# Optimization experiments

Measured on AMD Instinct MI355X. Metric: run time of the kernel, lower is better.

Reference implementation:

```python
import jax, jax.numpy as jnp
import numpy as np

EPS_BN = 1e-5
DIVERSITY_TEMP = 100.0  # lucidrains codebook_diversity_temperature default
COMMIT_W = 1.0
DIVERSITY_W = 1.0
ORTHO_W = 1.0


def conv1d(x, w, b=None, stride=1, pad=0):
    # x: [B,C,T], w: [O,I,K] (torch layout)
    y = jax.lax.conv_general_dilated(x, w, (stride,), [(pad, pad)],
                                     dimension_numbers=('NCH', 'OIH', 'NCH'))
    if b is not None:
        y = y + b[None, :, None]
    return y


def conv1d_transpose(x, w_torch, stride, pad):
    # torch ConvTranspose1d weight: (in, out, k). Equivalent input-dilated conv
    # with flipped kernel and padding k-1-pad.
    w = jnp.flip(jnp.transpose(w_torch, (1, 0, 2)), axis=2)  # -> (out,in,k)
    k = w.shape[2]
    p = k - 1 - pad
    return jax.lax.conv_general_dilated(x, w, (1,), [(p, p)],
                                        lhs_dilation=(stride,),
                                        dimension_numbers=('NCH', 'OIH', 'NCH'))


def batchnorm(x, g, b):
    # training-mode BatchNorm1d: stats over (batch, time) per channel
    m = x.mean(axis=(0, 2), keepdims=True)
    v = x.var(axis=(0, 2), keepdims=True)
    return (x - m) * jax.lax.rsqrt(v + EPS_BN) * g[None, :, None] + b[None, :, None]


def setup_inputs():
    key = jax.random.key(0)
    ks = jax.random.split(key, 10)
    f32 = jnp.float32
    rn = lambda k, shape, s: jax.random.normal(k, shape, f32) * s
    return {
        'x': jax.random.normal(ks[0], (8, 1, 24000), f32),
        # encoder: 1->16->32->64
        'w1': rn(ks[1], (16, 1, 5), 0.3), 'b1': jnp.zeros(16, f32),
        'g1': jnp.ones(16, f32), 'be1': jnp.zeros(16, f32),
        'w2': rn(ks[2], (32, 16, 5), 0.1), 'b2': jnp.zeros(32, f32),
        'g2': jnp.ones(32, f32), 'be2': jnp.zeros(32, f32),
        'w3': rn(ks[3], (64, 32, 25), 0.05), 'b3': jnp.zeros(64, f32),
        'g3': jnp.ones(64, f32), 'be3': jnp.zeros(64, f32),
        # VQ codebook [codebook_size=8192, dim=64]
        'embed': jax.random.normal(ks[4], (8192, 64), f32),
        # decoder
        'dw1': rn(ks[5], (64, 64, 25), 0.05),  # ConvTranspose1d weight (in,out,k)
        'dg1': jnp.ones(64, f32), 'dbe1': jnp.zeros(64, f32),
        'dw2': rn(ks[6], (64, 64, 5), 0.1), 'db2': jnp.zeros(64, f32),
        'dg2': jnp.ones(64, f32), 'dbe2': jnp.zeros(64, f32),
        'dw3': rn(ks[7], (1, 64, 1), 0.2), 'db3': jnp.zeros(1, f32),
        # fixed random subset for orthogonal reg (orthogonal_reg_max_codes=256)
        'ortho_idx': jax.random.randint(ks[8], (256,), 0, 8192),
    }


def reference(x, w1, b1, g1, be1, w2, b2, g2, be2, w3, b3, g3, be3,
              embed, dw1, dg1, dbe1, dw2, db2, dg2, dbe2, dw3, db3, ortho_idx):
    # ---- encoder ----
    h = batchnorm(jax.nn.silu(conv1d(x, w1, b1, 1, 2)), g1, be1)
    h = batchnorm(jax.nn.silu(conv1d(h, w2, b2, 1, 2)), g2, be2)
    z = batchnorm(jnp.tanh(conv1d(h, w3, b3, 12, 12)), g3, be3)  # [B,64,N]
    B, C, N = z.shape
    zf = jnp.transpose(z, (0, 2, 1)).reshape(B * N, C)  # [B*N, 64]

    # ---- VQ: nearest neighbor over codebook ----
    d2 = (jnp.sum(zf * zf, -1, keepdims=True) - 2.0 * (zf @ embed.T)
          + jnp.sum(embed * embed, -1)[None, :])          # [B*N, K]
    dist = jnp.sqrt(jnp.clip(d2, 1e-12))                  # euclidean (cdist p=2)
    idx = jnp.argmin(d2, axis=-1)                         # [B*N]
    q = embed[idx]                                        # codebook gather

    commit = jnp.mean((jax.lax.stop_gradient(q) - zf) ** 2)

    prob = jax.nn.softmax(-dist * DIVERSITY_TEMP, axis=-1)
    avg_prob = prob.mean(axis=0)                          # [K]
    diversity = jnp.sum(avg_prob * jnp.log(jnp.clip(avg_prob, 1e-30)))

    codes = embed[ortho_idx]                              # [256, 64]
    normed = codes * jax.lax.rsqrt(jnp.sum(codes * codes, -1, keepdims=True) + 1e-12)
    cos = normed @ normed.T
    n = codes.shape[0]
    ortho = jnp.sum(cos * cos) / (n * n) - 1.0 / n

    loss = COMMIT_W * commit + DIVERSITY_W * diversity + ORTHO_W * ortho

    # straight-through estimator
    q_st = zf + jax.lax.stop_gradient(q - zf)
    zq = jnp.transpose(q_st.reshape(B, N, C), (0, 2, 1))  # [B,64,N]

    # ---- decoder ----
    d = batchnorm(jax.nn.silu(conv1d_transpose(zq, dw1, 12, 12)), dg1, dbe1)
    d = batchnorm(jax.nn.silu(conv1d(d, dw2, db2, 1, 2)), dg2, dbe2)
    recon = conv1d(d, dw3, db3, 1, 0)

    T = x.shape[2]
    cur = recon.shape[2]
    if cur > T:
        recon = recon[:, :, :T]
    elif cur < T:
        recon = jnp.pad(recon, ((0, 0), (0, 0), (0, T - cur)))
    return recon, idx.reshape(B, N), loss, (commit, diversity, ortho)
```

## Files before the change

### kernel.cpp

```cpp
#include <hip/hip_runtime.h>
#include <math.h>
#include <float.h>

#define DEV __device__ __forceinline__

#define BB 8
#define TT 24000
#define TD 23989
#define NZ 2000
#define ROWS 16000
#define NE 8192
#define NCG 8

typedef __attribute__((ext_vector_type(8))) short bf16x8;
typedef __attribute__((ext_vector_type(4))) float f32x4;

__device__ double g_st[640];
__device__ double g_misc[2];
__device__ float  g_e2[NE];
__device__ float  g_avg[NE];
__device__ float  g_z2[ROWS];
__device__ float  g_rdm[ROWS];
__device__ int    g_rix[ROWS];
__device__ float  g_ob[256 * 64];
__device__ float  g_pmd[ROWS * NCG];
__device__ int    g_pmi[ROWS * NCG];
__device__ int    g_pcc[ROWS * NCG];
__device__ float2 g_cand[ROWS * 256];
__device__ unsigned short g_zbh[ROWS * 64], g_zbl[ROWS * 64];
__device__ unsigned short g_ebh[NE * 64],  g_ebl[NE * 64];
__device__ float  g_s1[16], g_sh1[16];
__device__ float  g_s2[32], g_sh2[32];
__device__ float  g_sd1[64], g_shd1[64];
__device__ float  g_w2f[2560];
__device__ float  g_b2f[32];
__device__ float  g_w3f[64 * 32 * 25];
__device__ float  g_b3f[64];
__device__ float  g_dw2f[64 * 5 * 64];
__device__ float  g_db2f[64];
__device__ float  g_dw1t[64 * 64 * 25];
__device__ float  g_zbn[ROWS * 64];
__device__ double g_zbnd[ROWS * 64];
__device__ float  g_zq[BB * 64 * NZ];
__device__ float  g_y1[BB * 16 * TT];
__device__ float  g_zpre[BB * 64 * NZ];
__device__ float  g_yd1[BB * 64 * TD];
__device__ float  g_y2[BB * 32 * TT];
__device__ float  g_yd2[BB * 64 * TD];

DEV float wsum(float v){
  #pragma unroll
  for (int o = 32; o; o >>= 1) v += __shfl_xor(v, o, 64);
  return v;
}
DEV int clampc(int c){ return c < 0 ? 0 : (c > NE - 1 ? NE - 1 : c); }
DEV float bss(unsigned short s){ union { unsigned u; float f; } v; v.u = ((unsigned)s) << 16; return v.f; }
DEV unsigned short f2bs(float f){
  union { float f; unsigned u; } v; v.f = f;
  unsigned r = (v.u + 0x7FFF + ((v.u >> 16) & 1)) >> 16;
  return (unsigned short)r;
}

__global__ void k_zero(){
  int i = blockIdx.x * 256 + threadIdx.x;
  if (i < 640) g_st[i] = 0.0;
  if (i < 2) g_misc[i] = 0.0;
  if (i < NE) g_avg[i] = 0.f;
}

__global__ void k_embprep(const float* __restrict__ embed){
  int gt = blockIdx.x * 256 + threadIdx.x;
  int gs = gridDim.x * 256;
  for (int i = gt; i < NE * 64; i += gs){
    float v = embed[i];
    unsigned short h = f2bs(v);
    g_ebh[i] = h;
    g_ebl[i] = f2bs(v - bss(h));
  }
  for (int c = gt; c < NE; c += gs){
    float s = 0.f;
    for (int j = 0; j < 64; j++){ float v = embed[c * 64 + j]; s += v * v; }
    g_e2[c] = s;
  }
}

__global__ void k_zsplit(){
  int i = blockIdx.x * 256 + threadIdx.x;
  if (i < ROWS * 64){
    float v = g_zbn[i];
    unsigned short h = f2bs(v);
    g_zbh[i] = h;
    g_zbl[i] = f2bs(v - bss(h));
  }
}

__global__ void k_conv1(const float* __restrict__ x, const float* __restrict__ w1,
                        const float* __restrict__ b1){
  int b = blockIdx.y, t0 = blockIdx.x * 256, tid = threadIdx.x;
  __shared__ float xs[260], wl[80], bl[16], sacc[16], qacc[16];
  if (tid < 80) wl[tid] = w1[tid];
  if (tid < 16){ bl[tid] = b1[tid]; sacc[tid] = 0.f; qacc[tid] = 0.f; }
  for (int i = tid; i < 260; i += 256){ int g = t0 - 2 + i; xs[i] = ((unsigned)g < TT) ? x[b * TT + g] : 0.f; }
  __syncthreads();
  int t = t0 + tid;
  bool ok = t < TT;
  float xv[5];
  #pragma unroll
  for (int k = 0; k < 5; k++) xv[k] = xs[tid + k];
  float out[16];
  #pragma unroll
  for (int c = 0; c < 16; c++){
    float a = bl[c];
    #pragma unroll
    for (int k = 0; k < 5; k++) a += wl[c * 5 + k] * xv[k];
    float o = ok ? a / (1.f + expf(-a)) : 0.f;
    out[c] = o;
    if (ok) g_y1[(b * 16 + c) * TT + t] = o;
  }
  int lane = tid & 63;
  #pragma unroll
  for (int c = 0; c < 16; c++){
    float s = wsum(out[c]);
    float q = wsum(out[c] * out[c]);
    if (lane == 0){ atomicAdd(&sacc[c], s); atomicAdd(&qacc[c], q); }
  }
  __syncthreads();
  if (tid < 16){ atomicAdd(&g_st[tid * 2], (double)sacc[tid]); atomicAdd(&g_st[tid * 2 + 1], (double)qacc[tid]); }
}

__global__ void k_fold2(const float* __restrict__ g1, const float* __restrict__ be1,
                        const float* __restrict__ w2, const float* __restrict__ b2){
  int tid = threadIdx.x;
  if (blockIdx.x == 0 && tid < 16){
    double m = g_st[tid * 2] / 192000.0, v = g_st[tid * 2 + 1] / 192000.0 - m * m;
    float s = g1[tid] / sqrtf((float)v + 1e-5f);
    g_s1[tid] = s; g_sh1[tid] = be1[tid] - (float)m * s;
  }
  if (blockIdx.x == 0 && tid < 32) g_b2f[tid] = b2[tid];
  int gt = blockIdx.x * 256 + tid;
  for (int i = gt; i < 2560; i += 8 * 256){
    int co = i & 31, r = i >> 5, k = r % 5, ci = r / 5;
    g_w2f[i] = w2[(co * 16 + ci) * 5 + k];
  }
}

__global__ void __launch_bounds__(256) k_conv2(){
  int b = blockIdx.y, t0 = blockIdx.x * 256, tid = threadIdx.x;
  __shared__ float xs[16][260];
  __shared__ float sacc[32], qacc[32];
  __shared__ float s1l[16], sh1l[16];
  int lane = tid & 63, wv = tid >> 6;
  int cb = wv * 8;
  if (tid < 32){ sacc[tid] = 0.f; qacc[tid] = 0.f; }
  if (tid < 16){ s1l[tid] = g_s1[tid]; sh1l[tid] = g_sh1[tid]; }
  __syncthreads();
  for (int i = tid; i < 16 * 260; i += 256){
    int ci = i / 260, tt = i - ci * 260, g = t0 - 2 + tt;
    xs[ci][tt] = ((unsigned)g < TT) ? (s1l[ci] * g_y1[(b * 16 + ci) * TT + g] + sh1l[ci]) : 0.f;
  }
  __syncthreads();
  float acc[4][8];
  #pragma unroll
  for (int j = 0; j < 4; j++)
    #pragma unroll
    for (int i = 0; i < 8; i++) acc[j][i] = g_b2f[cb + i];
  for (int ci = 0; ci < 16; ci++){
    #pragma unroll
    for (int k = 0; k < 5; k++){
      const float4* wp = (const float4*)(g_w2f + (ci * 5 + k) * 32 + cb);
      float4 w0 = wp[0], w1v = wp[1];
      float wr[8] = { w0.x, w0.y, w0.z, w0.w, w1v.x, w1v.y, w1v.z, w1v.w };
      #pragma unroll
      for (int j = 0; j < 4; j++){
        float xv = xs[ci][lane + 64 * j + k];
        #pragma unroll
        for (int i = 0; i < 8; i++) acc[j][i] += wr[i] * xv;
      }
    }
  }
  #pragma unroll
  for (int i = 0; i < 8; i++){
    int co = cb + i;
    float s = 0.f, q = 0.f;
    #pragma unroll
    for (int j = 0; j < 4; j++){
      int t = t0 + lane + 64 * j;
      bool ok = t < TT;
      float a = acc[j][i];
      float o = ok ? a / (1.f + expf(-a)) : 0.f;
      if (ok) g_y2[(b * 32 + co) * TT + t] = o;
      s += o; q += o * o;
    }
    s = wsum(s); q = wsum(q);
    if (lane == 0){ atomicAdd(&sacc[co], s); atomicAdd(&qacc[co], q); }
  }
  __syncthreads();
  if (tid < 32){ atomicAdd(&g_st[128 + tid * 2], (double)sacc[tid]); atomicAdd(&g_st[128 + tid * 2 + 1], (double)qacc[tid]); }
}

__global__ void k_fold3(const float* __restrict__ g2, const float* __restrict__ be2,
                        const float* __restrict__ w3, const float* __restrict__ b3){
  int tid = threadIdx.x;
  if (blockIdx.x == 0 && tid < 32){
    double m = g_st[128 + tid * 2] / 192000.0, v = g_st[128 + tid * 2 + 1] / 192000.0 - m * m;
    float s = g2[tid] / sqrtf((float)v + 1e-5f);
    g_s2[tid] = s; g_sh2[tid] = be2[tid] - (float)m * s;
  }
  if (blockIdx.x == 0 && tid >= 64 && tid < 128) g_b3f[tid - 64] = b3[tid - 64];
  int gt = blockIdx.x * 256 + tid;
  for (int i = gt; i < 64 * 32 * 25; i += 64 * 256){
    int co = i & 63, r = i >> 6, k = r % 25, ci = r / 25;
    g_w3f[i] = w3[(co * 32 + ci) * 25 + k];
  }
}

__global__ void __launch_bounds__(256) k_conv3(){
  __shared__ float xs[32][400];
  __shared__ float s2l[32], sh2l[32];
  int tid = threadIdx.x, b = blockIdx.y, t0 = blockIdx.x * 32;
  int lane = tid & 63, wv = tid >> 6;
  int cb = wv * 16;
  int tl = lane & 31, h = lane >> 5;
  if (tid < 32){ s2l[tid] = g_s2[tid]; sh2l[tid] = g_sh2[tid]; }
  __syncthreads();
  int p0 = t0 * 12 - 12;
  for (int i = tid; i < 32 * 397; i += 256){
    int ci = i / 397, pp = i - ci * 397, g = p0 + pp;
    xs[ci][pp] = ((unsigned)g < TT) ? (s2l[ci] * g_y2[(b * 32 + ci) * TT + g] + sh2l[ci]) : 0.f;
  }
  __syncthreads();
  float acc[16];
  #pragma unroll
  for (int i = 0; i < 16; i++) acc[i] = 0.f;
  for (int cii = 0; cii < 16; cii++){
    int ci = h * 16 + cii;
    #pragma unroll
    for (int k = 0; k < 25; k++){
      float xv = xs[ci][tl * 12 + k];
      const float4* wp = (const float4*)(g_w3f + (ci * 25 + k) * 64 + cb);
      float4 a0 = wp[0], a1 = wp[1], a2 = wp[2], a3 = wp[3];
      acc[0] += a0.x * xv; acc[1] += a0.y * xv; acc[2] += a0.z * xv; acc[3] += a0.w * xv;
      acc[4] += a1.x * xv; acc[5] += a1.y * xv; acc[6] += a1.z * xv; acc[7] += a1.w * xv;
      acc[8] += a2.x * xv; acc[9] += a2.y * xv; acc[10] += a2.z * xv; acc[11] += a2.w * xv;
      acc[12] += a3.x * xv; acc[13] += a3.y * xv; acc[14] += a3.z * xv; acc[15] += a3.w * xv;
    }
  }
  #pragma unroll
  for (int i = 0; i < 16; i++) acc[i] += __shfl_xor(acc[i], 32, 64);
  int t = t0 + tl;
  if (h == 0 && t < NZ){
    #pragma unroll
    for (int i = 0; i < 16; i++)
      g_zpre[(b * 64 + cb + i) * NZ + t] = tanhf(acc[i] + g_b3f[cb + i]);
  }
}

__global__ void k_stats(int which, int L, int stoff){
  const float* p = (which == 0) ? g_zpre : (which == 1) ? g_yd1 : g_yd2;
  int co = blockIdx.y, t0 = blockIdx.x * 256, tid = threadIdx.x;
  int t = t0 + tid;
  float s = 0.f, q = 0.f;
  if (t < L){
    for (int b = 0; b < BB; b++){ float v = p[(b * 64 + co) * L + t]; s += v; q += v * v; }
  }
  s = wsum(s); q = wsum(q);
  __shared__ float sa[4], qa[4];
  int w = tid >> 6, lane = tid & 63;
  if (lane == 0){ sa[w] = s; qa[w] = q; }
  __syncthreads();
  if (tid == 0){
    atomicAdd(&g_st[stoff + co * 2], (double)(sa[0] + sa[1] + sa[2] + sa[3]));
    atomicAdd(&g_st[stoff + co * 2 + 1], (double)(qa[0] + qa[1] + qa[2] + qa[3]));
  }
}

__global__ void k_zbn(const float* __restrict__ g3, const float* __restrict__ be3){
  __shared__ float tile[64][65];
  __shared__ float s3[64], sh3[64];
  __shared__ double s3d[64], sh3d[64];
  int tid = threadIdx.x, b = blockIdx.y, n0 = blockIdx.x * 64;
  if (tid < 64){
    double m = g_st[256 + tid * 2] / 16000.0, v = g_st[256 + tid * 2 + 1] / 16000.0 - m * m;
    double sd = (double)g3[tid] / sqrt(v + 1e-5);
    double shd = (double)be3[tid] - m * sd;
    s3d[tid] = sd; sh3d[tid] = shd;
    s3[tid] = (float)sd; sh3[tid] = (float)shd;
  }
  __syncthreads();
  for (int i = tid; i < 64 * 64; i += 256){
    int c = i >> 6, nn = i & 63, n = n0 + nn;
    tile[c][nn] = (n < NZ) ? (s3[c] * g_zpre[(b * 64 + c) * NZ + n] + sh3[c]) : 0.f;
  }
  __syncthreads();
  int lane = tid & 63;
  for (int it = 0; it < 16; ++it){
    int nn = (tid >> 6) + it * 4;
    int n = n0 + nn, c = lane;
    if (n < NZ){
      float v = tile[c][nn];
      int row = b * NZ + n;
      g_zbn[row * 64 + c] = v;
      g_zbnd[row * 64 + c] = s3d[c] * (double)g_zpre[(b * 64 + c) * NZ + n] + sh3d[c];
      float s = wsum(v * v);
      if (lane == 0) g_z2[row] = s;
    }
  }
}

__global__ void __launch_bounds__(256) k_vq1(){
  __shared__ unsigned short bsh[64 * 72];
  __shared__ unsigned short bsl[64 * 72];
  __shared__ float2 ring[64][16];
  __shared__ int cnt[64];
  int tid = threadIdx.x, lane = tid & 63, w = tid >> 6;
  int q = lane >> 4, col = lane & 15;
  int rowbase = blockIdx.x * 64 + w * 16;
  int cbase = blockIdx.y * 1024;
  int grp = blockIdx.y;
  if (tid < 64) cnt[tid] = 0;
  #pragma unroll
  for (int i = 0; i < 4; i++)
    ring[w * 16 + (lane & 15)][(lane >> 4) * 4 + i] = make_float2(FLT_MAX, __int_as_float(NE - 1));
  bf16x8 ah0, ah1, al0, al1;
  {
    const unsigned short* zh = g_zbh + (rowbase + col) * 64;
    const unsigned short* zl = g_zbl + (rowbase + col) * 64;
    ah0 = *(const bf16x8*)(zh + q * 8);
    ah1 = *(const bf16x8*)(zh + 32 + q * 8);
    al0 = *(const bf16x8*)(zl + q * 8);
    al1 = *(const bf16x8*)(zl + 32 + q * 8);
  }
  float z2r[4];
  #pragma unroll
  for (int r = 0; r < 4; r++) z2r[r] = g_z2[rowbase + q * 4 + r];
  float thr[4], lmin[4]; int lamc[4];
  #pragma unroll
  for (int r = 0; r < 4; r++){ thr[r] = FLT_MAX; lmin[r] = FLT_MAX; lamc[r] = NE - 1; }
  float runmin[4] = {FLT_MAX, FLT_MAX, FLT_MAX, FLT_MAX};
  for (int ch = 0; ch < 16; ++ch){
    __syncthreads();
    {
      int cl = tid >> 2, seg = tid & 3;
      int cglob = cbase + ch * 64 + cl;
      *(int4*)&bsh[cl * 72 + seg * 16]     = *(const int4*)(g_ebh + cglob * 64 + seg * 16);
      *(int4*)&bsh[cl * 72 + seg * 16 + 8] = *(const int4*)(g_ebh + cglob * 64 + seg * 16 + 8);
      *(int4*)&bsl[cl * 72 + seg * 16]     = *(const int4*)(g_ebl + cglob * 64 + seg * 16);
      *(int4*)&bsl[cl * 72 + seg * 16 + 8] = *(const int4*)(g_ebl + cglob * 64 + seg * 16 + 8);
    }
    __syncthreads();
    float d2s[4][4];
    float tmin[4] = {FLT_MAX, FLT_MAX, FLT_MAX, FLT_MAX};
    #pragma unroll
    for (int t = 0; t < 4; t++){
      int ct = cbase + ch * 64 + t * 16;
      const unsigned short* bhp = &bsh[(t * 16 + col) * 72];
      const unsigned short* blp = &bsl[(t * 16 + col) * 72];
      bf16x8 bh0 = *(const bf16x8*)(bhp + q * 8);
      bf16x8 bh1 = *(const bf16x8*)(bhp + 32 + q * 8);
      bf16x8 bl0 = *(const bf16x8*)(blp + q * 8);
      bf16x8 bl1 = *(const bf16x8*)(blp + 32 + q * 8);
      f32x4 acc = {0.f, 0.f, 0.f, 0.f};
      acc = __builtin_amdgcn_mfma_f32_16x16x32_bf16(al0, bh0, acc, 0, 0, 0);
      acc = __builtin_amdgcn_mfma_f32_16x16x32_bf16(al1, bh1, acc, 0, 0, 0);
      acc = __builtin_amdgcn_mfma_f32_16x16x32_bf16(ah0, bl0, acc, 0, 0, 0);
      acc = __builtin_amdgcn_mfma_f32_16x16x32_bf16(ah1, bl1, acc, 0, 0, 0);
      acc = __builtin_amdgcn_mfma_f32_16x16x32_bf16(ah0, bh0, acc, 0, 0, 0);
      acc = __builtin_amdgcn_mfma_f32_16x16x32_bf16(ah1, bh1, acc, 0, 0, 0);
      float e2c = g_e2[ct + col];
      #pragma unroll
      for (int r = 0; r < 4; r++){
        float d = z2r[r] + e2c - 2.f * acc[r];
        d2s[t][r] = d;
        if (d < lmin[r]){ lmin[r] = d; lamc[r] = ct + col; }
        tmin[r] = fminf(tmin[r], d);
      }
    }
    #pragma unroll
    for (int r = 0; r < 4; r++){
      float m = tmin[r];
      m = fminf(m, __shfl_xor(m, 1, 64));
      m = fminf(m, __shfl_xor(m, 2, 64));
      m = fminf(m, __shfl_xor(m, 4, 64));
      m = fminf(m, __shfl_xor(m, 8, 64));
      if (m < runmin[r]){
        runmin[r] = m;
        thr[r] = m + 0.71f * sqrtf(fmaxf(m, 0.f)) + 0.13f;
      }
    }
    #pragma unroll
    for (int t = 0; t < 4; t++){
      int ct = cbase + ch * 64 + t * 16;
      bool any = false;
      #pragma unroll
      for (int r = 0; r < 4; r++) if (d2s[t][r] < thr[r]) any = true;
      if (__ballot(any)){
        #pragma unroll
        for (int r = 0; r < 4; r++){
          if (d2s[t][r] < thr[r]){
            int lr = w * 16 + q * 4 + r;
            int s = atomicAdd(&cnt[lr], 1) & 15;
            ring[lr][s] = make_float2(sqrtf(fmaxf(d2s[t][r], 1e-12f)), __int_as_float(ct + col));
          }
        }
      }
    }
  }
  __syncthreads();
  #pragma unroll
  for (int r = 0; r < 4; r++){
    float m = lmin[r]; int c = lamc[r];
    #pragma unroll
    for (int o = 1; o <= 8; o <<= 1){
      float om = __shfl_xor(m, o, 64);
      int oc = __shfl_xor(c, o, 64);
      if (om < m || (om == m && oc < c)){ m = om; c = oc; }
    }
    if (col == 0){
      int gr = rowbase + q * 4 + r;
      g_pmd[gr * NCG + grp] = m;
      g_pmi[gr * NCG + grp] = c;
    }
  }
  if (lane < 16){
    int lr = w * 16 + lane;
    g_pcc[(rowbase + lane) * NCG + grp] = cnt[lr];
  }
  #pragma unroll
  for (int i = 0; i < 4; i++){
    int idx = lane * 4 + i;
    int lr = idx >> 4, s = idx & 15;
    g_cand[(rowbase + lr) * 256 + grp * 16 + s] = ring[w * 16 + lr][s];
  }
}

__global__ void k_vq1b(){
  int row = blockIdx.x * 256 + threadIdx.x;
  if (row >= ROWS) return;
  float best = FLT_MAX; int bi = NE - 1;
  for (int cg = 0; cg < NCG; ++cg){
    float d = g_pmd[row * NCG + cg]; int i = g_pmi[row * NCG + cg];
    if (d < best || (d == best && i < bi)){ best = d; bi = i; }
  }
  g_rdm[row] = sqrtf(fmaxf(best, 1e-12f));
  g_rix[row] = bi;
}

__global__ void __launch_bounds__(256) k_vq3(const float* __restrict__ embed,
                                             float* __restrict__ outIdx){
  __shared__ int   ccode[4][144];
  __shared__ float cdst[4][144];
  __shared__ int   cn[4];
  __shared__ double bsum[4];
  int w = threadIdx.x >> 6, lane = threadIdx.x & 63;
  int row = blockIdx.x * 4 + w;
  float dmin = g_rdm[row];
  int seedc = clampc(g_rix[row]);
  if (lane == 0){ cn[w] = 0; ccode[w][0] = seedc; }
  __syncthreads();
  if (lane == 0) cn[w] = 1;
  int grp = lane & 7;
  int sub = lane >> 3;
  int cnt = g_pcc[row * NCG + grp]; if (cnt > 16) cnt = 16;
  int s0 = sub * 2, s1 = s0 + 2; if (s1 > cnt) s1 = cnt;
  for (int s = s0; s < s1; ++s){
    float2 cd = g_cand[row * 256 + grp * 16 + s];
    float dist = cd.x; int c = clampc(__float_as_int(cd.y));
    if (dist <= dmin + 0.353f && c != seedc){
      int i = atomicAdd(&cn[w], 1);
      ccode[w][i] = c;
    }
  }
  __syncthreads();
  int n = cn[w];
  double zdl = g_zbnd[row * 64 + lane];
  double bd = DBL_MAX; int bc = NE - 1;
  for (int i = 0; i < n; i++){
    int c = ccode[w][i];
    double diff = zdl - (double)embed[c * 64 + lane];
    double d = diff * diff;
    #pragma unroll
    for (int o = 32; o; o >>= 1) d += __shfl_xor(d, o, 64);
    if (lane == 0) cdst[w][i] = (float)d;
    if (d < bd || (d == bd && c < bc)){ bd = d; bc = c; }
  }
  __syncthreads();
  float dminE = (float)sqrt(bd);
  float Zp = 0.f;
  for (int i = lane; i < n; i += 64)
    Zp += expf(-100.f * (sqrtf(cdst[w][i]) - dminE));
  float Z = fmaxf(wsum(Zp), 1e-30f);
  if (lane == 0){
    g_rix[row] = bc;
    outIdx[row] = (float)bc;
    bsum[w] = bd;
  }
  for (int i = lane; i < n; i += 64)
    atomicAdd(&g_avg[ccode[w][i]], expf(-100.f * (sqrtf(cdst[w][i]) - dminE)) / Z);
  __syncthreads();
  if (threadIdx.x == 0)
    atomicAdd(&g_misc[0], bsum[0] + bsum[1] + bsum[2] + bsum[3]);
}

__global__ void k_orthoprep(const float* __restrict__ embed, const int* __restrict__ oidx){
  int tid = threadIdx.x;
  int c = clampc(oidx[tid]);
  float s = 0.f;
  for (int j = 0; j < 64; j++){ float v = embed[c * 64 + j]; s += v * v; }
  float r = 1.f / sqrtf(s + 1e-12f);
  for (int j = 0; j < 64; j++) g_ob[tid * 64 + j] = embed[c * 64 + j] * r;
}

__global__ void k_ortho(){
  int w = threadIdx.x >> 6, lane = threadIdx.x & 63;
  int i = blockIdx.x * 4 + w;
  float acc = 0.f;
  for (int j = lane; j < 256; j += 64){
    float d = 0.f;
    for (int k = 0; k < 64; k++) d += g_ob[i * 64 + k] * g_ob[j * 64 + k];
    acc += d * d;
  }
  acc = wsum(acc);
  if (lane == 0) atomicAdd(&g_misc[1], (double)acc);
}

__global__ void k_div(float* __restrict__ outS){
  int tid = threadIdx.x;
  double part = 0.0;
  for (int c = tid; c < NE; c += 256){
    double p = (double)g_avg[c] / 16000.0;
    double pc = p < 1e-30 ? 1e-30 : p;
    part += p * log(pc);
  }
  __shared__ double red[256];
  red[tid] = part; __syncthreads();
  for (int o = 128; o; o >>= 1){ if (tid < o) red[tid] += red[tid + o]; __syncthreads(); }
  if (tid == 0){
    double diversity = red[0];
    double commit = g_misc[0] / (double)(ROWS * 64);
    double ortho = g_misc[1] / 65536.0 - 1.0 / 256.0;
    double loss = commit + diversity + ortho;
    outS[0] = (float)loss;
    outS[1] = (float)commit;
    outS[2] = (float)diversity;
    outS[3] = (float)ortho;
  }
}

__global__ void k_zq(const float* __restrict__ embed){
  __shared__ float tile[64][65];
  int tid = threadIdx.x, b = blockIdx.y, n0 = blockIdx.x * 64;
  for (int i = tid; i < 64 * 64; i += 256){
    int nn = i >> 6, c = i & 63;
    int n = n0 + nn;
    int code = (n < NZ) ? clampc(g_rix[b * NZ + n]) : 0;
    tile[c][nn] = embed[code * 64 + c];
  }
  __syncthreads();
  for (int i = tid; i < 64 * 64; i += 256){
    int c = i >> 6, nn = i & 63;
    int n = n0 + nn;
    if (n < NZ) g_zq[(b * 64 + c) * NZ + n] = tile[c][nn];
  }
}

__global__ void k_folddw1(const float* __restrict__ dw1){
  int gt = blockIdx.x * 256 + threadIdx.x;
  for (int i = gt; i < 64 * 64 * 25; i += 100 * 256){
    int co = i & 63, r = i >> 6, k = r % 25, ci = r / 25;
    g_dw1t[i] = dw1[(ci * 64 + co) * 25 + (24 - k)];
  }
}

__global__ void __launch_bounds__(256, 3) k_dconv1(){
  __shared__ float xsd[16][260];
  __shared__ float wsh[4][64][28];
  __shared__ float sacc[4], qacc[4];
  int tid = threadIdx.x, b = blockIdx.y;
  int cb = blockIdx.z * 4;
  int t0 = blockIdx.x * 3072;
  int nb = blockIdx.x * 256 - 1;
  int w = tid >> 6, lane = tid & 63;
  if (tid < 4){ sacc[tid] = 0.f; qacc[tid] = 0.f; }
  for (int i = tid; i < 6400; i += 256){
    int c = i & 3, r = i >> 2;
    int k = r % 25, ci = r / 25;
    wsh[c][ci][k] = g_dw1t[r * 64 + cb + c];
  }
  float acc[4][12];
  #pragma unroll
  for (int q = 0; q < 4; q++)
    #pragma unroll
    for (int p = 0; p < 12; p++) acc[q][p] = 0.f;
  for (int cc = 0; cc < 4; ++cc){
    __syncthreads();
    for (int i = tid; i < 16 * 259; i += 256){
      int ci = i / 259, nl = i - ci * 259;
      int n = nb + nl;
      xsd[ci][nl] = ((unsigned)n < NZ) ? g_zq[(b * 64 + cc * 16 + ci) * NZ + n] : 0.f;
    }
    __syncthreads();
    #pragma unroll 2
    for (int ci = 0; ci < 16; ++ci){
      int cia = cc * 16 + ci;
      const float4* xp = (const float4*)&xsd[ci][4 * lane];
      float4 xA = xp[0], xB = xp[1];
      float xv[6] = { xA.x, xA.y, xA.z, xA.w, xB.x, xB.y };
      const float4* wp = (const float4*)&wsh[w][cia][0];
      float4 w0 = wp[0], w1 = wp[1], w2 = wp[2], w3 = wp[3], w4 = wp[4], w5 = wp[5];
      float wv[25] = { w0.x, w0.y, w0.z, w0.w, w1.x, w1.y, w1.z, w1.w,
                       w2.x, w2.y, w2.z, w2.w, w3.x, w3.y, w3.z, w3.w,
                       w4.x, w4.y, w4.z, w4.w, w5.x, w5.y, w5.z, w5.w,
                       wsh[w][cia][24] };
      #pragma unroll
      for (int q = 0; q < 4; ++q){
        acc[q][0] += wv[0] * xv[q];
        acc[q][0] += wv[12] * xv[q + 1];
        acc[q][0] += wv[24] * xv[q + 2];
        #pragma unroll
        for (int p = 1; p < 12; ++p){
          acc[q][p] += wv[12 - p] * xv[q + 1];
          acc[q][p] += wv[24 - p] * xv[q + 2];
        }
      }
    }
  }
  bool full = (t0 + 3072 <= TD);
  float s = 0.f, qs = 0.f;
  float* dst = &g_yd1[(b * 64 + cb + w) * TD + t0 + lane * 48];
  #pragma unroll
  for (int q = 0; q < 4; ++q){
    float o[12];
    #pragma unroll
    for (int p = 0; p < 12; ++p){
      int t = t0 + lane * 48 + q * 12 + p;
      float a = acc[q][p];
      float v = (t < TD) ? a / (1.f + expf(-a)) : 0.f;
      o[p] = v; s += v; qs += v * v;
    }
    if (full){
      ((float4*)(dst + q * 12))[0] = make_float4(o[0], o[1], o[2], o[3]);
      ((float4*)(dst + q * 12))[1] = make_float4(o[4], o[5], o[6], o[7]);
      ((float4*)(dst + q * 12))[2] = make_float4(o[8], o[9], o[10], o[11]);
    } else {
      #pragma unroll
      for (int p = 0; p < 12; ++p){
        int t = t0 + lane * 48 + q * 12 + p;
        if (t < TD) dst[q * 12 + p] = o[p];
      }
    }
  }
  s = wsum(s); qs = wsum(qs);
  if (lane == 0){ atomicAdd(&sacc[w], s); atomicAdd(&qacc[w], qs); }
  __syncthreads();
  if (tid < 4){
    atomicAdd(&g_st[384 + (cb + tid) * 2], (double)sacc[tid]);
    atomicAdd(&g_st[384 + (cb + tid) * 2 + 1], (double)qacc[tid]);
  }
}

__global__ void k_foldd2(const float* __restrict__ dg1, const float* __restrict__ dbe1,
                         const float* __restrict__ dw2, const float* __restrict__ db2){
  int tid = threadIdx.x;
  if (blockIdx.x == 0 && tid < 64){
    double m = g_st[384 + tid * 2] / 191912.0, v = g_st[384 + tid * 2 + 1] / 191912.0 - m * m;
    float sc = dg1[tid] / sqrtf((float)v + 1e-5f);
    g_sd1[tid] = sc; g_shd1[tid] = dbe1[tid] - (float)m * sc;
    g_db2f[tid] = db2[tid];
  }
  int gt = blockIdx.x * 256 + tid;
  for (int i = gt; i < 64 * 5 * 64; i += 32 * 256){
    int co = i & 63, r = i >> 6, k = r % 5, ci = r / 5;
    g_dw2f[i] = dw2[(co * 64 + ci) * 5 + k];
  }
}

__global__ void __launch_bounds__(256, 2) k_dconv2(){
  __shared__ float xs[16][772];
  __shared__ float wch[16 * 5 * 32];
  __shared__ float sdl[64], shdl[64];
  __shared__ float sacc[32], qacc[32];
  int tid = threadIdx.x, b = blockIdx.y, bz = blockIdx.z;
  int t0 = blockIdx.x * 768;
  int lane = tid & 63, wv = tid >> 6;
  int cb = bz * 32 + wv * 8;
  if (tid < 64){ sdl[tid] = g_sd1[tid]; shdl[tid] = g_shd1[tid]; }
  if (tid < 32){ sacc[tid] = 0.f; qacc[tid] = 0.f; }
  float acc[12][8];
  #pragma unroll
  for (int j = 0; j < 12; j++)
    #pragma unroll
    for (int i = 0; i < 8; i++) acc[j][i] = g_db2f[cb + i];
  for (int ch = 0; ch < 4; ++ch){
    __syncthreads();
    for (int i = tid; i < 16 * 772; i += 256){
      int ci = i / 772, tt = i - ci * 772, g = t0 - 2 + tt;
      int cia = ch * 16 + ci;
      xs[ci][tt] = ((unsigned)g < TD) ? (sdl[cia] * g_yd1[(b * 64 + cia) * TD + g] + shdl[cia]) : 0.f;
    }
    for (int i = tid; i < 2560; i += 256){
      int r = i >> 5, c = i & 31;
      wch[i] = g_dw2f[(ch * 80 + r) * 64 + bz * 32 + c];
    }
    __syncthreads();
    for (int ci = 0; ci < 16; ++ci){
      float xv[3][8];
      #pragma unroll
      for (int j4 = 0; j4 < 3; ++j4){
        const float4* xp = (const float4*)&xs[ci][j4 * 256 + 4 * lane];
        float4 a = xp[0], bq = xp[1];
        xv[j4][0] = a.x;  xv[j4][1] = a.y;  xv[j4][2] = a.z;  xv[j4][3] = a.w;
        xv[j4][4] = bq.x; xv[j4][5] = bq.y; xv[j4][6] = bq.z; xv[j4][7] = bq.w;
      }
      #pragma unroll
      for (int k = 0; k < 5; ++k){
        const float4* wp = (const float4*)(wch + (ci * 5 + k) * 32 + wv * 8);
        float4 w0 = wp[0], w1 = wp[1];
        float wr[8] = { w0.x, w0.y, w0.z, w0.w, w1.x, w1.y, w1.z, w1.w };
        #pragma unroll
        for (int j4 = 0; j4 < 3; ++j4){
          #pragma unroll
          for (int jj = 0; jj < 4; ++jj){
            float xvv = xv[j4][jj + k];
            #pragma unroll
            for (int i = 0; i < 8; i++) acc[j4 * 4 + jj][i] += wr[i] * xvv;
          }
        }
      }
    }
  }
  bool full = (t0 + 768 <= TD);
  #pragma unroll
  for (int i = 0; i < 8; i++){
    int co = cb + i;
    float s = 0.f, q = 0.f;
    float* dst = &g_yd2[(b * 64 + co) * TD + t0 + lane * 4];
    #pragma unroll
    for (int j4 = 0; j4 < 3; ++j4){
      float o[4];
      #pragma unroll
      for (int jj = 0; jj < 4; ++jj){
        int t = t0 + j4 * 256 + lane * 4 + jj;
        float a = acc[j4 * 4 + jj][i];
        float v = (t < TD) ? a / (1.f + expf(-a)) : 0.f;
        o[jj] = v; s += v; q += v * v;
      }
      if (full){
        *(float4*)(dst + j4 * 256) = make_float4(o[0], o[1], o[2], o[3]);
      } else {
        #pragma unroll
        for (int jj = 0; jj < 4; ++jj){
          int t = t0 + j4 * 256 + lane * 4 + jj;
          if (t < TD) dst[j4 * 256 + jj] = o[jj];
        }
      }
    }
    s = wsum(s); q = wsum(q);
    if (lane == 0){ atomicAdd(&sacc[wv * 8 + i], s); atomicAdd(&qacc[wv * 8 + i], q); }
  }
  __syncthreads();
  if (tid < 32){
    int co = bz * 32 + tid;
    atomicAdd(&g_st[512 + co * 2], (double)sacc[tid]);
    atomicAdd(&g_st[512 + co * 2 + 1], (double)qacc[tid]);
  }
}

__global__ void k_recon(const float* __restrict__ dg2, const float* __restrict__ dbe2,
                        const float* __restrict__ dw3, const float* __restrict__ db3,
                        float* __restrict__ outR){
  __shared__ float wf[64];
  __shared__ float bsh2;
  int tid = threadIdx.x, b = blockIdx.y, t0 = blockIdx.x * 256;
  if (tid < 64){
    double m = g_st[512 + tid * 2] / 191912.0, v = g_st[512 + tid * 2 + 1] / 191912.0 - m * m;
    float sc = dg2[tid] / sqrtf((float)v + 1e-5f);
    float shv = dbe2[tid] - (float)m * sc;
    wf[tid] = dw3[tid] * sc;
    float contrib = wsum(dw3[tid] * shv);
    if (tid == 0) bsh2 = db3[0] + contrib;
  }
  __syncthreads();
  int t = t0 + tid;
  if (t < TT){
    if (t < TD){
      float a = bsh2;
      for (int ci = 0; ci < 64; ci++) a += wf[ci] * g_yd2[(b * 64 + ci) * TD + t];
      outR[b * TT + t] = a;
    } else {
      outR[b * TT + t] = 0.f;
    }
  }
}

extern "C" void kernel_launch(void* const* d_in, const int* in_sizes, int n_in,
                              void* d_out, int out_size, void* d_ws, size_t ws_size,
                              hipStream_t stream){
  (void)in_sizes; (void)n_in; (void)out_size; (void)d_ws; (void)ws_size;
  const float* x    = (const float*)d_in[0];
  const float* w1   = (const float*)d_in[1];
  const float* b1   = (const float*)d_in[2];
  const float* g1   = (const float*)d_in[3];
  const float* be1  = (const float*)d_in[4];
  const float* w2   = (const float*)d_in[5];
  const float* b2   = (const float*)d_in[6];
  const float* g2   = (const float*)d_in[7];
  const float* be2  = (const float*)d_in[8];
  const float* w3   = (const float*)d_in[9];
  const float* b3   = (const float*)d_in[10];
  const float* g3   = (const float*)d_in[11];
  const float* be3  = (const float*)d_in[12];
  const float* embed= (const float*)d_in[13];
  const float* dw1  = (const float*)d_in[14];
  const float* dg1  = (const float*)d_in[15];
  const float* dbe1 = (const float*)d_in[16];
  const float* dw2  = (const float*)d_in[17];
  const float* db2  = (const float*)d_in[18];
  const float* dg2  = (const float*)d_in[19];
  const float* dbe2 = (const float*)d_in[20];
  const float* dw3  = (const float*)d_in[21];
  const float* db3  = (const float*)d_in[22];
  const int* oidx   = (const int*)d_in[23];

  float* out    = (float*)d_out;
  float* outIdx = out + 192000;
  float* outS   = out + 208000;

  hipLaunchKernelGGL(k_zero, dim3(32), dim3(256), 0, stream);
  hipLaunchKernelGGL(k_embprep, dim3(64), dim3(256), 0, stream, embed);
  hipLaunchKernelGGL(k_conv1, dim3(94, 8), dim3(256), 0, stream, x, w1, b1);
  hipLaunchKernelGGL(k_fold2, dim3(8), dim3(256), 0, stream, g1, be1, w2, b2);
  hipLaunchKernelGGL(k_conv2, dim3(94, 8), dim3(256), 0, stream);
  hipLaunchKernelGGL(k_fold3, dim3(64), dim3(256), 0, stream, g2, be2, w3, b3);
  hipLaunchKernelGGL(k_conv3, dim3(63, 8), dim3(256), 0, stream);
  hipLaunchKernelGGL(k_stats, dim3(8, 64), dim3(256), 0, stream, 0, NZ, 256);
  hipLaunchKernelGGL(k_zbn, dim3(32, 8), dim3(256), 0, stream, g3, be3);
  hipLaunchKernelGGL(k_zsplit, dim3(4000), dim3(256), 0, stream);
  hipLaunchKernelGGL(k_vq1, dim3(250, 8), dim3(256), 0, stream);
  hipLaunchKernelGGL(k_vq1b, dim3(63), dim3(256), 0, stream);
  hipLaunchKernelGGL(k_vq3, dim3(4000), dim3(256), 0, stream, embed, outIdx);
  hipLaunchKernelGGL(k_orthoprep, dim3(1), dim3(256), 0, stream, embed, oidx);
  hipLaunchKernelGGL(k_ortho, dim3(64), dim3(256), 0, stream);
  hipLaunchKernelGGL(k_div, dim3(1), dim3(256), 0, stream, outS);
  hipLaunchKernelGGL(k_zq, dim3(32, 8), dim3(256), 0, stream, embed);
  hipLaunchKernelGGL(k_folddw1, dim3(100), dim3(256), 0, stream, dw1);
  hipLaunchKernelGGL(k_dconv1, dim3(8, 8, 16), dim3(256), 0, stream);
  hipLaunchKernelGGL(k_foldd2, dim3(32), dim3(256), 0, stream, dg1, dbe1, dw2, db2);
  hipLaunchKernelGGL(k_dconv2, dim3(32, 8, 2), dim3(256), 0, stream);
  hipLaunchKernelGGL(k_recon, dim3(94, 8), dim3(256), 0, stream, dg2, dbe2, dw3, db3, out);
}
```

Measured before the change: 862.2 us.

## Double-buffer k_dconv2 input and weight tiles with register prefetch

Restructures the decoder conv2 kernel so input channels are staged in chunks of 8 into two shared-memory buffers. The next chunk is loaded from global memory into registers while the current chunk is computed. This hides global load latency behind the FMA loop and drops one barrier per chunk. It adds 30 prefetch registers on top of a 96-float accumulator under launch_bounds(256,2), which risks spills or lower occupancy, and it doubles the number of chunk iterations.

```diff
diff --git a/kernel.cpp b/kernel.cpp
--- a/kernel.cpp
+++ b/kernel.cpp
@@ -675,8 +675,8 @@
 }
 
 __global__ void __launch_bounds__(256, 2) k_dconv2(){
-  __shared__ float xs[16][772];
-  __shared__ float wch[16 * 5 * 32];
+  __shared__ float xs[2][8][772];
+  __shared__ float wch[2][1280];
   __shared__ float sdl[64], shdl[64];
   __shared__ float sacc[32], qacc[32];
   int tid = threadIdx.x, b = blockIdx.y, bz = blockIdx.z;
@@ -685,35 +685,79 @@
   int cb = bz * 32 + wv * 8;
   if (tid < 64){ sdl[tid] = g_sd1[tid]; shdl[tid] = g_shd1[tid]; }
   if (tid < 32){ sacc[tid] = 0.f; qacc[tid] = 0.f; }
+  __syncthreads();
+
   float acc[12][8];
   #pragma unroll
   for (int j = 0; j < 12; j++)
     #pragma unroll
     for (int i = 0; i < 8; i++) acc[j][i] = g_db2f[cb + i];
-  for (int ch = 0; ch < 4; ++ch){
-    __syncthreads();
-    for (int i = tid; i < 16 * 772; i += 256){
-      int ci = i / 772, tt = i - ci * 772, g = t0 - 2 + tt;
-      int cia = ch * 16 + ci;
-      xs[ci][tt] = ((unsigned)g < TD) ? (sdl[cia] * g_yd1[(b * 64 + cia) * TD + g] + shdl[cia]) : 0.f;
-    }
-    for (int i = tid; i < 2560; i += 256){
+
+  bool okj[3];
+  #pragma unroll
+  for (int j = 0; j < 3; j++) okj[j] = (unsigned)(t0 - 2 + tid + 256 * j) < TD;
+  int ecia_l = tid >> 2;
+  int eg = t0 - 2 + 768 + (tid & 3);
+  bool oke = (unsigned)eg < TD;
+
+  float pfx[25];
+  float pfw[5];
+
+  auto PREF = [&](int hc){
+    #pragma unroll
+    for (int ci = 0; ci < 8; ++ci){
+      const float* rowp = g_yd1 + (size_t)(b * 64 + hc * 8 + ci) * TD;
+      #pragma unroll
+      for (int j = 0; j < 3; ++j){
+        int g = t0 - 2 + tid + 256 * j;
+        pfx[ci * 3 + j] = rowp[okj[j] ? g : 0];
+      }
+    }
+    if (tid < 32)
+      pfx[24] = g_yd1[(size_t)(b * 64 + hc * 8 + ecia_l) * TD + (oke ? eg : 0)];
+    #pragma unroll
+    for (int j = 0; j < 5; ++j){
+      int i = tid + 256 * j;
       int r = i >> 5, c = i & 31;
-      wch[i] = g_dw2f[(ch * 80 + r) * 64 + bz * 32 + c];
-    }
-    __syncthreads();
-    for (int ci = 0; ci < 16; ++ci){
+      pfw[j] = g_dw2f[(hc * 40 + r) * 64 + bz * 32 + c];
+    }
+  };
+  auto WRITE = [&](int buf, int hc){
+    #pragma unroll
+    for (int ci = 0; ci < 8; ++ci){
+      int cia = hc * 8 + ci;
+      float s = sdl[cia], sh = shdl[cia];
+      #pragma unroll
+      for (int j = 0; j < 3; ++j)
+        xs[buf][ci][tid + 256 * j] = okj[j] ? (s * pfx[ci * 3 + j] + sh) : 0.f;
+    }
+    if (tid < 32){
+      int cia = hc * 8 + ecia_l;
+      xs[buf][ecia_l][768 + (tid & 3)] = oke ? (sdl[cia] * pfx[24] + shdl[cia]) : 0.f;
+    }
+    #pragma unroll
+    for (int j = 0; j < 5; ++j)
+      wch[buf][tid + 256 * j] = pfw[j];
+  };
+
+  PREF(0);
+  WRITE(0, 0);
+  __syncthreads();
+  for (int hc = 0; hc < 8; ++hc){
+    int cur = hc & 1;
+    if (hc < 7) PREF(hc + 1);
+    for (int ci = 0; ci < 8; ++ci){
       float xv[3][8];
       #pragma unroll
       for (int j4 = 0; j4 < 3; ++j4){
-        const float4* xp = (const float4*)&xs[ci][j4 * 256 + 4 * lane];
+        const float4* xp = (const float4*)&xs[cur][ci][j4 * 256 + 4 * lane];
         float4 a = xp[0], bq = xp[1];
         xv[j4][0] = a.x;  xv[j4][1] = a.y;  xv[j4][2] = a.z;  xv[j4][3] = a.w;
         xv[j4][4] = bq.x; xv[j4][5] = bq.y; xv[j4][6] = bq.z; xv[j4][7] = bq.w;
       }
       #pragma unroll
       for (int k = 0; k < 5; ++k){
-        const float4* wp = (const float4*)(wch + (ci * 5 + k) * 32 + wv * 8);
+        const float4* wp = (const float4*)(&wch[cur][(ci * 5 + k) * 32 + wv * 8]);
         float4 w0 = wp[0], w1 = wp[1];
         float wr[8] = { w0.x, w0.y, w0.z, w0.w, w1.x, w1.y, w1.z, w1.w };
         #pragma unroll
@@ -727,7 +771,10 @@
         }
       }
     }
-  }
+    if (hc < 7) WRITE(cur ^ 1, hc + 1);
+    __syncthreads();
+  }
+
   bool full = (t0 + 768 <= TD);
   #pragma unroll
   for (int i = 0; i < 8; i++){
```

Measured after the change: 856.1 us. About the same (-0.7%).
